# Kernel tuning notes

Measured on AMD Instinct MI355X. Metric: run time of the kernel, lower is better.

## Reference

```python
import jax, jax.numpy as jnp
import numpy as np

NB = 2        # trm_num_blocks
H = 4         # trm_num_heads
D = 128       # trm_hidden_dim
L = 512
B = 1
PAD = 0
NEG = jnp.float32(-2**32 + 1)


def _ln(x, g, b, eps=1e-8):
    m = x.mean(-1, keepdims=True)
    v = x.var(-1, keepdims=True)
    return (x - m) / jnp.sqrt(v + eps) * g + b


def setup_inputs() -> dict:
    key = jax.random.key(0)
    ks = jax.random.split(key, 16)
    s = 0.02
    inp = {
        "log_seqs": jax.random.randint(ks[0], (B, L), 0, 1000),
        "seqs": jax.random.normal(ks[1], (B, L, D), jnp.float32),
        "time_matrix_K": jax.random.normal(ks[2], (B, L, L, D), jnp.float32),
        # per-block stacked params [NB, ...]
        "Wq": jax.random.normal(ks[3], (NB, D, D), jnp.float32) * s,
        "bq": jnp.zeros((NB, D), jnp.float32),
        "Wk": jax.random.normal(ks[4], (NB, D, D), jnp.float32) * s,
        "bk": jnp.zeros((NB, D), jnp.float32),
        "Wv": jax.random.normal(ks[5], (NB, D, D), jnp.float32) * s,
        "bv": jnp.zeros((NB, D), jnp.float32),
        "Wt": jax.random.normal(ks[6], (NB, D, D), jnp.float32) * s,
        "bt": jnp.zeros((NB, D), jnp.float32),
        "Wtp": jax.random.normal(ks[7], (NB, D, 1), jnp.float32) * s,
        "btp": jnp.zeros((NB, 1), jnp.float32),
        "ln1_g": jnp.ones((NB, D), jnp.float32),
        "ln1_b": jnp.zeros((NB, D), jnp.float32),
        "ln2_g": jnp.ones((NB, D), jnp.float32),
        "ln2_b": jnp.zeros((NB, D), jnp.float32),
        "W1": jax.random.normal(ks[8], (NB, D, D), jnp.float32) * s,
        "b1": jnp.zeros((NB, D), jnp.float32),
        "W2": jax.random.normal(ks[9], (NB, D, D), jnp.float32) * s,
        "b2": jnp.zeros((NB, D), jnp.float32),
        "lnf_g": jnp.ones((D,), jnp.float32),
        "lnf_b": jnp.zeros((D,), jnp.float32),
    }
    return inp


def reference(log_seqs, seqs, time_matrix_K, Wq, bq, Wk, bk, Wv, bv, Wt, bt,
              Wtp, btp, ln1_g, ln1_b, ln2_g, ln2_b, W1, b1, W2, b2, lnf_g, lnf_b):
    hd = D // H
    pad = (log_seqs == PAD)                     # [B, L] True at padding
    keep = (~pad)[..., None].astype(seqs.dtype)  # [B, L, 1]
    seqs = seqs * keep
    causal = ~jnp.tril(jnp.ones((L, L), bool))  # True above diagonal (masked)
    # combined mask [1, B, L, L]: pad query rows OR non-causal entries
    mask = pad[None, :, :, None] | causal[None, None, :, :]

    attn_ws = []
    for i in range(NB):
        Q = _ln(seqs, ln1_g[i], ln1_b[i])
        q = Q @ Wq[i] + bq[i]
        k = seqs @ Wk[i] + bk[i]
        v = seqs @ Wv[i] + bv[i]
        # head-major layout [H, B, L, hd] (matches torch split+cat along dim 0)
        qh = q.reshape(B, L, H, hd).transpose(2, 0, 1, 3)
        kh = k.reshape(B, L, H, hd).transpose(2, 0, 1, 3)
        vh = v.reshape(B, L, H, hd).transpose(2, 0, 1, 3)
        scores = jnp.einsum('hbqd,hbkd->hbqk', qh, kh)  # [H, B, L, L]
        # time bias: sigmoid(proj(relu(W_t t))) in (0,1); log is negative
        tw = jax.nn.sigmoid(
            (jax.nn.relu(time_matrix_K @ Wt[i] + bt[i]) @ Wtp[i] + btp[i]).squeeze(-1)
        )                                             # [B, L, L]
        scores = (scores + jnp.log(tw)) / jnp.float32(hd) ** 0.5
        scores = jnp.where(mask, NEG, scores)
        w = jax.nn.softmax(scores, axis=-1)           # dropout is identity (eval)
        attn_ws.append(w.reshape(H * B, L, L))
        out = jnp.einsum('hbqk,hbkd->hbqd', w, vh).transpose(1, 2, 0, 3).reshape(B, L, D)
        seqs = Q + out
        x = _ln(seqs, ln2_g[i], ln2_b[i])
        y = jax.nn.relu(x @ W1[i] + b1[i]) @ W2[i] + b2[i]
        seqs = (x + y) * keep                         # FFN residual adds post-LN x
    log_feats = _ln(seqs, lnf_g, lnf_b)
    return (log_feats, tuple(attn_ws))
```

## Files before the change

### kernel.cpp

```cpp
#include <hip/hip_runtime.h>

#define L 512
#define D 128
#define H 4
#define HD 32
#define XLD 132
#define NTB 576

typedef __bf16 bf16x8 __attribute__((ext_vector_type(8)));
typedef float  f32x4  __attribute__((ext_vector_type(4)));

__device__ __forceinline__ unsigned short bfbits(float v){
  __bf16 h = (__bf16)v; unsigned short u; __builtin_memcpy(&u, &h, 2); return u;
}
__device__ __forceinline__ bf16x8 cvt8(float4 a0, float4 a1){
  bf16x8 r;
  r[0] = (__bf16)a0.x; r[1] = (__bf16)a0.y; r[2] = (__bf16)a0.z; r[3] = (__bf16)a0.w;
  r[4] = (__bf16)a1.x; r[5] = (__bf16)a1.y; r[6] = (__bf16)a1.z; r[7] = (__bf16)a1.w;
  return r;
}

__device__ __forceinline__ void write_qA(unsigned short* qA, int row, int c, float v){
  int qt = row >> 4, m = row & 15;
  int h = c >> 5, cc = c & 31;
  qA[(((qt * 4 + h) * 64) + (cc >> 3) * 16 + m) * 8 + (cc & 7)] = bfbits(v);
}
__device__ __forceinline__ void write_kB(unsigned short* kB, int row, int c, float v){
  int h = c >> 5, cc = c & 31;
  int nt = row >> 4;
  kB[((h * 32 + nt) * 64 + (cc >> 3) * 16 + (row & 15)) * 8 + (cc & 7)] = bfbits(v);
}
__device__ __forceinline__ void write_vB(unsigned short* vB, int row, int c, float v){
  int h = c >> 5, cc = c & 31;
  int kk = row >> 5, qv = (row >> 3) & 3, jv = row & 7;
  int nt = cc >> 4;
  vB[(((h * 16 + kk) * 2 + nt) * 64 + qv * 16 + (cc & 15)) * 8 + jv] = bfbits(v);
}

__device__ __forceinline__ void row_stats16(const float (*buf)[XLD], int tid,
                                            float* mean_s, float* rstd_s){
  int row_l = tid >> 4, seg = tid & 15;
  const float* p = &buf[row_l][seg * 8];
  float4 f0 = *(const float4*)p, f1 = *(const float4*)(p + 4);
  float sum = f0.x + f0.y + f0.z + f0.w + f1.x + f1.y + f1.z + f1.w;
  float sq  = f0.x*f0.x + f0.y*f0.y + f0.z*f0.z + f0.w*f0.w
            + f1.x*f1.x + f1.y*f1.y + f1.z*f1.z + f1.w*f1.w;
#pragma unroll
  for (int o = 1; o < 16; o <<= 1){ sum += __shfl_xor(sum, o); sq += __shfl_xor(sq, o); }
  if (seg == 0){
    float mn = sum * (1.f / 128.f);
    mean_s[row_l] = mn;
    rstd_s[row_l] = rsqrtf(fmaxf(sq * (1.f / 128.f) - mn * mn, 0.f) + 1e-8f);
  }
}

__device__ __forceinline__ void build_afr(const float (*buf)[XLD], int lane, bf16x8* afr){
  int m = lane & 15, quad = lane >> 4;
#pragma unroll
  for (int k0 = 0; k0 < 4; ++k0){
    const float* p = &buf[m][k0 * 32 + quad * 8];
    afr[k0] = cvt8(*(const float4*)p, *(const float4*)(p + 4));
  }
}
__device__ __forceinline__ void build_afr_ln(const float (*buf)[XLD], int lane,
    const float* mean_s, const float* rstd_s,
    const float* __restrict__ g, const float* __restrict__ b, bf16x8* afr){
  int m = lane & 15, quad = lane >> 4;
  float mn = mean_s[m], rs = rstd_s[m];
#pragma unroll
  for (int k0 = 0; k0 < 4; ++k0){
    int c0 = k0 * 32 + quad * 8;
    const float* p = &buf[m][c0];
    float4 a0 = *(const float4*)p, a1 = *(const float4*)(p + 4);
    float q[8];
    q[0]=(a0.x-mn)*rs*g[c0+0]+b[c0+0]; q[1]=(a0.y-mn)*rs*g[c0+1]+b[c0+1];
    q[2]=(a0.z-mn)*rs*g[c0+2]+b[c0+2]; q[3]=(a0.w-mn)*rs*g[c0+3]+b[c0+3];
    q[4]=(a1.x-mn)*rs*g[c0+4]+b[c0+4]; q[5]=(a1.y-mn)*rs*g[c0+5]+b[c0+5];
    q[6]=(a1.z-mn)*rs*g[c0+6]+b[c0+6]; q[7]=(a1.w-mn)*rs*g[c0+7]+b[c0+7];
    bf16x8 r;
    r[0]=(__bf16)q[0]; r[1]=(__bf16)q[1]; r[2]=(__bf16)q[2]; r[3]=(__bf16)q[3];
    r[4]=(__bf16)q[4]; r[5]=(__bf16)q[5]; r[6]=(__bf16)q[6]; r[7]=(__bf16)q[7];
    afr[k0] = r;
  }
}

__global__ void k_prep(const float* __restrict__ Wt,
                       const float* __restrict__ Wq, const float* __restrict__ Wk,
                       const float* __restrict__ Wv, const float* __restrict__ W1,
                       const float* __restrict__ W2,
                       unsigned short* __restrict__ bfg, unsigned short* __restrict__ wf){
  int idx = blockIdx.x * 256 + threadIdx.x;
  if (idx < 32768){
    int jj   = idx & 7;
    int lane = (idx >> 3) & 63;
    int k0   = (idx >> 9) & 3;
    int nt   = idx >> 11;
    int d    = k0 * 32 + (lane >> 4) * 8 + jj;
    int col  = (nt & 7) * 16 + (lane & 15);
    int blk  = nt >> 3;
    bfg[idx] = bfbits(Wt[blk * D * D + d * D + col]);
  } else {
    int i2 = idx - 32768;
    int jj = i2 & 7, lane = (i2 >> 3) & 63, k0 = (i2 >> 9) & 3, nt = (i2 >> 11) & 7;
    int mat = i2 >> 14;
    int blk = mat / 5, m5 = mat % 5;
    const float* W = (m5 == 0 ? Wq : m5 == 1 ? Wk : m5 == 2 ? Wv : m5 == 3 ? W1 : W2)
                     + blk * D * D;
    int d = k0 * 32 + (lane >> 4) * 8 + jj;
    int col = nt * 16 + (lane & 15);
    wf[i2] = bfbits(W[d * D + col]);
  }
}

__global__ __launch_bounds__(256, 2) void k_tb_qkv(
    const float* __restrict__ T, const unsigned short* __restrict__ bfg,
    const float* __restrict__ bt, const float* __restrict__ wtp,
    const float* __restrict__ btp, float* __restrict__ logtw,
    const float* __restrict__ src, const int* __restrict__ ls,
    const float* __restrict__ g1, const float* __restrict__ b1,
    const unsigned short* __restrict__ wf,
    const float* __restrict__ bq, const float* __restrict__ bk,
    const float* __restrict__ bv,
    float* __restrict__ Q, unsigned short* __restrict__ qA,
    unsigned short* __restrict__ kB, unsigned short* __restrict__ vB){
  __shared__ __align__(16) unsigned short bsh[16384];
  __shared__ float bts[128], wtps[128];
  __shared__ float xs[16][XLD];
  __shared__ float mean_s[16], rstd_s[16];
  __shared__ float g1s[128], b1s[128];
  int tid = threadIdx.x;
  int lane = tid & 63, w = tid >> 6;
  int quad = lane >> 4;

  if (blockIdx.x < NTB){
    int m = lane & 15;
    const bf16x8* bls = (const bf16x8*)bsh;
    int strip = blockIdx.x * 4 + w;
    int b = 0;
#pragma unroll
    for (int i = 1; i < 8; ++i) if (strip >= 32 * i * (i + 1)) b = i;
    int r0 = strip - 32 * b * (b + 1);
    int q  = b * 64 + r0 / (b + 1);
    int kb = (r0 % (b + 1)) * 64;
    int wbase = q * L + kb;

    bf16x8 afr[4][4];
#pragma unroll
    for (int mt = 0; mt < 4; ++mt){
      const float* tp = T + (size_t)(wbase + mt * 16 + m) * D + quad * 8;
#pragma unroll
      for (int k0 = 0; k0 < 4; ++k0){
        float4 f0 = *(const float4*)(tp + k0 * 32);
        float4 f1 = *(const float4*)(tp + k0 * 32 + 4);
        afr[mt][k0] = cvt8(f0, f1);
      }
    }

#pragma unroll
    for (int blk = 0; blk < 2; ++blk){
      if (blk) __syncthreads();
      {
        const uint4* g = (const uint4*)(bfg + blk * 16384);
        uint4* s = (uint4*)bsh;
#pragma unroll
        for (int i = 0; i < 8; ++i) s[tid + i * 256] = g[tid + i * 256];
        if (tid < 128){ bts[tid] = bt[blk * 128 + tid]; wtps[tid] = wtp[blk * 128 + tid]; }
      }
      __syncthreads();

      f32x4 rs[4] = {{0,0,0,0},{0,0,0,0},{0,0,0,0},{0,0,0,0}};
#pragma unroll
      for (int ntl = 0; ntl < 8; ++ntl){
        f32x4 acc[4] = {{0,0,0,0},{0,0,0,0},{0,0,0,0},{0,0,0,0}};
#pragma unroll
        for (int k0 = 0; k0 < 4; ++k0){
          bf16x8 bfr = bls[(ntl * 4 + k0) * 64 + lane];
#pragma unroll
          for (int mt = 0; mt < 4; ++mt)
            acc[mt] = __builtin_amdgcn_mfma_f32_16x16x32_bf16(afr[mt][k0], bfr, acc[mt], 0, 0, 0);
        }
        float btv = bts[ntl * 16 + m];
        float wtv = wtps[ntl * 16 + m];
#pragma unroll
        for (int mt = 0; mt < 4; ++mt)
#pragma unroll
          for (int r = 0; r < 4; ++r)
            rs[mt][r] += fmaxf(acc[mt][r] + btv, 0.f) * wtv;
      }
#pragma unroll
      for (int mt = 0; mt < 4; ++mt)
#pragma unroll
        for (int r = 0; r < 4; ++r){
          float v = rs[mt][r];
          v += __shfl_xor(v, 1); v += __shfl_xor(v, 2);
          v += __shfl_xor(v, 4); v += __shfl_xor(v, 8);
          rs[mt][r] = v;
        }
      if (m == 0){
        float bp = btp[blk];
        float* out = logtw + blk * (L * L);
#pragma unroll
        for (int mt = 0; mt < 4; ++mt){
          float4 o;
          float s0 = rs[mt][0] + bp; o.x = -__logf(1.f + __expf(-s0));
          float s1 = rs[mt][1] + bp; o.y = -__logf(1.f + __expf(-s1));
          float s2 = rs[mt][2] + bp; o.z = -__logf(1.f + __expf(-s2));
          float s3 = rs[mt][3] + bp; o.w = -__logf(1.f + __expf(-s3));
          *(float4*)(out + wbase + mt * 16 + quad * 4) = o;
        }
      }
    }
    return;
  }

  int bi = blockIdx.x - NTB;
  int rowbase = (bi & 31) * 16;
  int mat = bi >> 5;
  int row_l = tid >> 4, seg = tid & 15;

  const float* sp = src + (rowbase + row_l) * D + seg * 8;
  float4 f0 = *(const float4*)sp, f1 = *(const float4*)(sp + 4);
  if (ls[rowbase + row_l] == 0){
    f0 = make_float4(0,0,0,0); f1 = make_float4(0,0,0,0);
  }
  *(float4*)&xs[row_l][seg * 8] = f0;
  *(float4*)&xs[row_l][seg * 8 + 4] = f1;
  if (mat == 0 && tid < 128){ g1s[tid] = g1[tid]; b1s[tid] = b1[tid]; }
  __syncthreads();
  if (mat == 0){
    row_stats16(xs, tid, mean_s, rstd_s);
    __syncthreads();
    float mn = mean_s[row_l], rs = rstd_s[row_l];
    float* qp = Q + (rowbase + row_l) * D + seg * 8;
    float4 o0, o1;
    int c0 = seg * 8;
    o0.x=(f0.x-mn)*rs*g1s[c0+0]+b1s[c0+0]; o0.y=(f0.y-mn)*rs*g1s[c0+1]+b1s[c0+1];
    o0.z=(f0.z-mn)*rs*g1s[c0+2]+b1s[c0+2]; o0.w=(f0.w-mn)*rs*g1s[c0+3]+b1s[c0+3];
    o1.x=(f1.x-mn)*rs*g1s[c0+4]+b1s[c0+4]; o1.y=(f1.y-mn)*rs*g1s[c0+5]+b1s[c0+5];
    o1.z=(f1.z-mn)*rs*g1s[c0+6]+b1s[c0+6]; o1.w=(f1.w-mn)*rs*g1s[c0+7]+b1s[c0+7];
    *(float4*)qp = o0; *(float4*)(qp + 4) = o1;
  }

  int mcol = lane & 15;
  bf16x8 afr[4];
  if (mat == 0) build_afr_ln(xs, lane, mean_s, rstd_s, g1s, b1s, afr);
  else          build_afr(xs, lane, afr);

  const float* bias_v = (mat == 0 ? bq : mat == 1 ? bk : bv);
#pragma unroll
  for (int jl = 0; jl < 2; ++jl){
    int nt = w * 2 + jl;
    const bf16x8* wfb = (const bf16x8*)wf + ((size_t)mat * 8 + nt) * 4 * 64;
    f32x4 acc = {0, 0, 0, 0};
#pragma unroll
    for (int k0 = 0; k0 < 4; ++k0)
      acc = __builtin_amdgcn_mfma_f32_16x16x32_bf16(afr[k0], wfb[k0 * 64 + lane], acc, 0, 0, 0);
    int c = nt * 16 + mcol;
    float bias = bias_v[c];
#pragma unroll
    for (int r = 0; r < 4; ++r){
      int row = rowbase + quad * 4 + r;
      float v = acc[r] + bias;
      if (mat == 0) write_qA(qA, row, c, v);
      else if (mat == 1) write_kB(kB, row, c, v);
      else write_vB(vB, row, c, v);
    }
  }
}

__global__ __launch_bounds__(256) void k_attn(
    const unsigned short* __restrict__ qA, const unsigned short* __restrict__ kB,
    const unsigned short* __restrict__ vB, const float* __restrict__ logtw,
    const int* __restrict__ ls, const float* __restrict__ Q,
    float* __restrict__ wout, float* __restrict__ xr){
  __shared__ __align__(16) unsigned short pa[16 * 64 * 8];
  __shared__ float pvp[4][2][64][4];
  __shared__ float smax[4][16], ssum[4][16];
  int qt = blockIdx.x >> 2, h = blockIdx.x & 3;
  int tid = threadIdx.x, lane = tid & 63, w = tid >> 6;
  int quad = lane >> 4, mcol = lane & 15;
  const float RS = 0.17677669529663687f;
  int row_max = qt * 16 + 15;
  bool skipw = (w * 128) > row_max;

  float e[8][4];
  if (!skipw){
    bf16x8 qf = ((const bf16x8*)qA)[(qt * 4 + h) * 64 + lane];
    f32x4 acc[8];
#pragma unroll
    for (int nt8 = 0; nt8 < 8; ++nt8){
      bf16x8 bf = ((const bf16x8*)kB)[(h * 32 + w * 8 + nt8) * 64 + lane];
      f32x4 z = {0, 0, 0, 0};
      acc[nt8] = __builtin_amdgcn_mfma_f32_16x16x32_bf16(qf, bf, z, 0, 0, 0);
    }
#pragma unroll
    for (int nt8 = 0; nt8 < 8; ++nt8){
      int col = w * 128 + nt8 * 16 + mcol;
#pragma unroll
      for (int r = 0; r < 4; ++r){
        int row = qt * 16 + quad * 4 + r;
        float sv = (acc[nt8][r] + logtw[row * L + col]) * RS;
        e[nt8][r] = (col <= row) ? sv : -3e38f;
      }
    }
  } else {
#pragma unroll
    for (int nt8 = 0; nt8 < 8; ++nt8)
#pragma unroll
      for (int r = 0; r < 4; ++r) e[nt8][r] = -3e38f;
  }

  float mx4[4] = {-3e38f, -3e38f, -3e38f, -3e38f};
#pragma unroll
  for (int nt8 = 0; nt8 < 8; ++nt8)
#pragma unroll
    for (int r = 0; r < 4; ++r) mx4[r] = fmaxf(mx4[r], e[nt8][r]);
#pragma unroll
  for (int r = 0; r < 4; ++r){
    float v = mx4[r];
    v = fmaxf(v, __shfl_xor(v, 1)); v = fmaxf(v, __shfl_xor(v, 2));
    v = fmaxf(v, __shfl_xor(v, 4)); v = fmaxf(v, __shfl_xor(v, 8));
    mx4[r] = v;
  }
  if (mcol == 0){
#pragma unroll
    for (int r = 0; r < 4; ++r) smax[w][quad * 4 + r] = mx4[r];
  }
  __syncthreads();
  float mxr[4], sum4[4] = {0, 0, 0, 0};
#pragma unroll
  for (int r = 0; r < 4; ++r){
    int rr = quad * 4 + r;
    mxr[r] = fmaxf(fmaxf(smax[0][rr], smax[1][rr]), fmaxf(smax[2][rr], smax[3][rr]));
  }
#pragma unroll
  for (int nt8 = 0; nt8 < 8; ++nt8)
#pragma unroll
    for (int r = 0; r < 4; ++r){
      float sv = e[nt8][r];
      float ev = (sv > -1e38f) ? __expf(sv - mxr[r]) : 0.f;
      e[nt8][r] = ev;
      sum4[r] += ev;
    }
#pragma unroll
  for (int r = 0; r < 4; ++r){
    float v = sum4[r];
    v += __shfl_xor(v, 1); v += __shfl_xor(v, 2);
    v += __shfl_xor(v, 4); v += __shfl_xor(v, 8);
    sum4[r] = v;
  }
  if (mcol == 0){
#pragma unroll
    for (int r = 0; r < 4; ++r) ssum[w][quad * 4 + r] = sum4[r];
  }
  __syncthreads();
  float inv[4]; int padr[4];
#pragma unroll
  for (int r = 0; r < 4; ++r){
    int rr = quad * 4 + r;
    inv[r] = 1.f / (ssum[0][rr] + ssum[1][rr] + ssum[2][rr] + ssum[3][rr]);
    padr[r] = (ls[qt * 16 + rr] == 0);
  }
#pragma unroll
  for (int nt8 = 0; nt8 < 8; ++nt8){
    int col = w * 128 + nt8 * 16 + mcol;
    int kk = col >> 5, qk = (col >> 3) & 3, jj = col & 7;
#pragma unroll
    for (int r = 0; r < 4; ++r){
      int rl = quad * 4 + r;
      float wv = padr[r] ? (1.f / 512.f) : e[nt8][r] * inv[r];
      wout[h * (L * L) + (qt * 16 + rl) * L + col] = wv;
      if (!skipw) pa[(kk * 64 + qk * 16 + rl) * 8 + jj] = bfbits(wv);
    }
  }

  f32x4 pacc[2] = {{0,0,0,0},{0,0,0,0}};
  if (!skipw){
#pragma unroll
    for (int kk4 = 0; kk4 < 4; ++kk4){
      int kk = w * 4 + kk4;
      bf16x8 af = ((const bf16x8*)pa)[kk * 64 + lane];
#pragma unroll
      for (int nt = 0; nt < 2; ++nt){
        bf16x8 bf = ((const bf16x8*)vB)[((h * 16 + kk) * 2 + nt) * 64 + lane];
        pacc[nt] = __builtin_amdgcn_mfma_f32_16x16x32_bf16(af, bf, pacc[nt], 0, 0, 0);
      }
    }
  }
#pragma unroll
  for (int nt = 0; nt < 2; ++nt)
#pragma unroll
    for (int r = 0; r < 4; ++r) pvp[w][nt][lane][r] = pacc[nt][r];
  __syncthreads();
  if (w < 2){
    int nt = w;
#pragma unroll
    for (int r = 0; r < 4; ++r){
      float o = pvp[0][nt][lane][r] + pvp[1][nt][lane][r]
              + pvp[2][nt][lane][r] + pvp[3][nt][lane][r];
      int row = qt * 16 + quad * 4 + r;
      int cg = h * HD + nt * 16 + mcol;
      xr[row * D + cg] = Q[row * D + cg] + o;
    }
  }
}

__global__ __launch_bounds__(256) void k_ffn_m(
    const float* __restrict__ xr, const int* __restrict__ ls,
    const float* __restrict__ g2, const float* __restrict__ b2,
    const unsigned short* __restrict__ wf, int mat1,
    const float* __restrict__ b1f, const float* __restrict__ b2f,
    int fuse_qkv, const float* __restrict__ g1, const float* __restrict__ b1,
    int matq, const float* __restrict__ bq, const float* __restrict__ bk,
    const float* __restrict__ bv,
    float* __restrict__ Q, unsigned short* __restrict__ qA,
    unsigned short* __restrict__ kB, unsigned short* __restrict__ vB,
    int fuse_lnf, const float* __restrict__ lg, const float* __restrict__ lb,
    float* __restrict__ lf){
  __shared__ float xs[16][XLD];
  __shared__ float x2s[16][XLD];
  __shared__ float y1s[16][XLD];
  __shared__ float xos[16][XLD];
  __shared__ float mean_s[16], rstd_s[16];
  __shared__ float gs[128], bs[128];
  int tid = threadIdx.x, rowbase = blockIdx.x * 16;
  int row_l = tid >> 4, seg = tid & 15;
  int lane = tid & 63, w = tid >> 6;
  int quad = lane >> 4, mcol = lane & 15;

  {
    const float* sp = xr + (rowbase + row_l) * D + seg * 8;
    *(float4*)&xs[row_l][seg * 8] = *(const float4*)sp;
    *(float4*)&xs[row_l][seg * 8 + 4] = *(const float4*)(sp + 4);
    if (tid < 128){ gs[tid] = g2[tid]; bs[tid] = b2[tid]; }
  }
  __syncthreads();
  row_stats16(xs, tid, mean_s, rstd_s);
  __syncthreads();
  {
    float mn = mean_s[row_l], rs = rstd_s[row_l];
#pragma unroll
    for (int i = 0; i < 8; ++i){
      int c = seg * 8 + i;
      x2s[row_l][c] = (xs[row_l][c] - mn) * rs * gs[c] + bs[c];
    }
  }
  __syncthreads();

  bf16x8 afr[4];
  build_afr(x2s, lane, afr);
#pragma unroll
  for (int jl = 0; jl < 2; ++jl){
    int nt = w * 2 + jl;
    const bf16x8* wfb = (const bf16x8*)wf + ((size_t)mat1 * 8 + nt) * 4 * 64;
    f32x4 acc = {0, 0, 0, 0};
#pragma unroll
    for (int k0 = 0; k0 < 4; ++k0)
      acc = __builtin_amdgcn_mfma_f32_16x16x32_bf16(afr[k0], wfb[k0 * 64 + lane], acc, 0, 0, 0);
    int c = nt * 16 + mcol;
    float bias = b1f[c];
#pragma unroll
    for (int r = 0; r < 4; ++r)
      y1s[quad * 4 + r][c] = fmaxf(acc[r] + bias, 0.f);
  }
  __syncthreads();

  build_afr(y1s, lane, afr);
#pragma unroll
  for (int jl = 0; jl < 2; ++jl){
    int nt = w * 2 + jl;
    const bf16x8* wfb = (const bf16x8*)wf + ((size_t)(mat1 + 1) * 8 + nt) * 4 * 64;
    f32x4 acc = {0, 0, 0, 0};
#pragma unroll
    for (int k0 = 0; k0 < 4; ++k0)
      acc = __builtin_amdgcn_mfma_f32_16x16x32_bf16(afr[k0], wfb[k0 * 64 + lane], acc, 0, 0, 0);
    int c = nt * 16 + mcol;
    float bias = b2f[c];
#pragma unroll
    for (int r = 0; r < 4; ++r){
      int rl = quad * 4 + r;
      float kp = (ls[rowbase + rl] != 0) ? 1.f : 0.f;
      xos[rl][c] = (x2s[rl][c] + acc[r] + bias) * kp;
    }
  }
  __syncthreads();

  if (fuse_qkv){
    if (tid < 128){ gs[tid] = g1[tid]; bs[tid] = b1[tid]; }
    row_stats16(xos, tid, mean_s, rstd_s);
    __syncthreads();
    {
      float mn = mean_s[row_l], rs = rstd_s[row_l];
      float* qp = Q + (rowbase + row_l) * D + seg * 8;
      float4 o0, o1;
      int c0 = seg * 8;
      o0.x=(xos[row_l][c0+0]-mn)*rs*gs[c0+0]+bs[c0+0];
      o0.y=(xos[row_l][c0+1]-mn)*rs*gs[c0+1]+bs[c0+1];
      o0.z=(xos[row_l][c0+2]-mn)*rs*gs[c0+2]+bs[c0+2];
      o0.w=(xos[row_l][c0+3]-mn)*rs*gs[c0+3]+bs[c0+3];
      o1.x=(xos[row_l][c0+4]-mn)*rs*gs[c0+4]+bs[c0+4];
      o1.y=(xos[row_l][c0+5]-mn)*rs*gs[c0+5]+bs[c0+5];
      o1.z=(xos[row_l][c0+6]-mn)*rs*gs[c0+6]+bs[c0+6];
      o1.w=(xos[row_l][c0+7]-mn)*rs*gs[c0+7]+bs[c0+7];
      *(float4*)qp = o0; *(float4*)(qp + 4) = o1;
    }
    bf16x8 afrQ[4], afrX[4];
    build_afr_ln(xos, lane, mean_s, rstd_s, gs, bs, afrQ);
    build_afr(xos, lane, afrX);
#pragma unroll
    for (int jl = 0; jl < 6; ++jl){
      int j = w * 6 + jl;
      int mat = j >> 3, nt = j & 7;
      const bf16x8* wfb = (const bf16x8*)wf + ((size_t)(matq + mat) * 8 + nt) * 4 * 64;
      f32x4 acc = {0, 0, 0, 0};
#pragma unroll
      for (int k0 = 0; k0 < 4; ++k0)
        acc = __builtin_amdgcn_mfma_f32_16x16x32_bf16(mat == 0 ? afrQ[k0] : afrX[k0],
                                                      wfb[k0 * 64 + lane], acc, 0, 0, 0);
      int c = nt * 16 + mcol;
      float bias = (mat == 0 ? bq : mat == 1 ? bk : bv)[c];
#pragma unroll
      for (int r = 0; r < 4; ++r){
        int row = rowbase + quad * 4 + r;
        float v = acc[r] + bias;
        if (mat == 0) write_qA(qA, row, c, v);
        else if (mat == 1) write_kB(kB, row, c, v);
        else write_vB(vB, row, c, v);
      }
    }
  }

  if (fuse_lnf){
    if (tid < 128){ gs[tid] = lg[tid]; bs[tid] = lb[tid]; }
    row_stats16(xos, tid, mean_s, rstd_s);
    __syncthreads();
    float mn = mean_s[row_l], rs = rstd_s[row_l];
    float* op = lf + (rowbase + row_l) * D + seg * 8;
    float4 o0, o1;
    int c0 = seg * 8;
    o0.x=(xos[row_l][c0+0]-mn)*rs*gs[c0+0]+bs[c0+0];
    o0.y=(xos[row_l][c0+1]-mn)*rs*gs[c0+1]+bs[c0+1];
    o0.z=(xos[row_l][c0+2]-mn)*rs*gs[c0+2]+bs[c0+2];
    o0.w=(xos[row_l][c0+3]-mn)*rs*gs[c0+3]+bs[c0+3];
    o1.x=(xos[row_l][c0+4]-mn)*rs*gs[c0+4]+bs[c0+4];
    o1.y=(xos[row_l][c0+5]-mn)*rs*gs[c0+5]+bs[c0+5];
    o1.z=(xos[row_l][c0+6]-mn)*rs*gs[c0+6]+bs[c0+6];
    o1.w=(xos[row_l][c0+7]-mn)*rs*gs[c0+7]+bs[c0+7];
    *(float4*)op = o0; *(float4*)(op + 4) = o1;
  }
}

extern "C" void kernel_launch(void* const* d_in, const int* in_sizes, int n_in,
                              void* d_out, int out_size, void* d_ws, size_t ws_size,
                              hipStream_t stream){
  const int*   ls   = (const int*)d_in[0];
  const float* seqs = (const float*)d_in[1];
  const float* T    = (const float*)d_in[2];
  const float* Wq   = (const float*)d_in[3];
  const float* bq   = (const float*)d_in[4];
  const float* Wk   = (const float*)d_in[5];
  const float* bk   = (const float*)d_in[6];
  const float* Wv   = (const float*)d_in[7];
  const float* bv   = (const float*)d_in[8];
  const float* Wt   = (const float*)d_in[9];
  const float* bt   = (const float*)d_in[10];
  const float* Wtp  = (const float*)d_in[11];
  const float* btp  = (const float*)d_in[12];
  const float* g1   = (const float*)d_in[13];
  const float* b1   = (const float*)d_in[14];
  const float* g2   = (const float*)d_in[15];
  const float* b2   = (const float*)d_in[16];
  const float* W1   = (const float*)d_in[17];
  const float* b1f  = (const float*)d_in[18];
  const float* W2   = (const float*)d_in[19];
  const float* b2f  = (const float*)d_in[20];
  const float* lg   = (const float*)d_in[21];
  const float* lb   = (const float*)d_in[22];

  float* ws    = (float*)d_ws;
  float* Q     = ws;
  float* xr    = Q + 65536;
  float* logtw = xr + 65536;
  unsigned short* bfg = (unsigned short*)(logtw + 2 * 262144);
  unsigned short* wf  = bfg + 32768;
  unsigned short* qA  = wf + 163840;
  unsigned short* kB  = qA + 65536;
  unsigned short* vB  = kB + 65536;

  float* outF = (float*)d_out;
  float* lf = outF;
  float* w0 = outF + 65536;
  float* w1 = w0 + 1048576;

  k_prep  <<<768, 256, 0, stream>>>(Wt, Wq, Wk, Wv, W1, W2, bfg, wf);
  k_tb_qkv<<<NTB + 96, 256, 0, stream>>>(T, bfg, bt, Wtp, btp, logtw,
                                         seqs, ls, g1, b1, wf, bq, bk, bv,
                                         Q, qA, kB, vB);
  k_attn<<<128, 256, 0, stream>>>(qA, kB, vB, logtw, ls, Q, w0, xr);
  k_ffn_m<<<32, 256, 0, stream>>>(xr, ls, g2, b2, wf, 3, b1f, b2f,
                                  1, g1 + D, b1 + D, 5, bq + D, bk + D, bv + D,
                                  Q, qA, kB, vB,
                                  0, lg, lb, lf);
  k_attn<<<128, 256, 0, stream>>>(qA, kB, vB, logtw + L * L, ls, Q, w1, xr);
  k_ffn_m<<<32, 256, 0, stream>>>(xr, ls, g2 + D, b2 + D, wf, 8, b1f + D, b2f + D,
                                  0, g1, b1, 0, bq, bk, bv,
                                  Q, qA, kB, vB,
                                  1, lg, lb, lf);
}
```

Measured before the change: 267.3 us.

## Fuse all stages into one persistent kernel with software grid barriers

```diff
diff --git a/kernel.cpp b/kernel.cpp
--- a/kernel.cpp
+++ b/kernel.cpp
@@ -5,7 +5,7 @@
 #define H 4
 #define HD 32
 #define XLD 132
-#define NTB 576
+#define NBLK 512
 
 typedef __bf16 bf16x8 __attribute__((ext_vector_type(8)));
 typedef float  f32x4  __attribute__((ext_vector_type(4)));
@@ -18,6 +18,27 @@
   r[0] = (__bf16)a0.x; r[1] = (__bf16)a0.y; r[2] = (__bf16)a0.z; r[3] = (__bf16)a0.w;
   r[4] = (__bf16)a1.x; r[5] = (__bf16)a1.y; r[6] = (__bf16)a1.z; r[7] = (__bf16)a1.w;
   return r;
+}
+
+__device__ __forceinline__ void gridbar(unsigned* cnt, unsigned* gen){
+  __threadfence();
+  __syncthreads();
+  if (threadIdx.x == 0){
+    unsigned g = __hip_atomic_load(gen, __ATOMIC_RELAXED, __HIP_MEMORY_SCOPE_AGENT);
+    unsigned arr = __hip_atomic_fetch_add(cnt, 1u, __ATOMIC_ACQ_REL, __HIP_MEMORY_SCOPE_AGENT);
+    if (arr == NBLK - 1u){
+      __hip_atomic_store(cnt, 0u, __ATOMIC_RELAXED, __HIP_MEMORY_SCOPE_AGENT);
+      __hip_atomic_fetch_add(gen, 1u, __ATOMIC_ACQ_REL, __HIP_MEMORY_SCOPE_AGENT);
+    } else {
+      unsigned t = 0;
+      while (__hip_atomic_load(gen, __ATOMIC_ACQUIRE, __HIP_MEMORY_SCOPE_AGENT) == g){
+        __builtin_amdgcn_s_sleep(2);
+        if (++t > (1u << 28)) break;
+      }
+    }
+  }
+  __syncthreads();
+  __threadfence();
 }
 
 __device__ __forceinline__ void write_qA(unsigned short* qA, int row, int c, float v){
@@ -84,140 +105,28 @@
   }
 }
 
-__global__ void k_prep(const float* __restrict__ Wt,
-                       const float* __restrict__ Wq, const float* __restrict__ Wk,
-                       const float* __restrict__ Wv, const float* __restrict__ W1,
-                       const float* __restrict__ W2,
-                       unsigned short* __restrict__ bfg, unsigned short* __restrict__ wf){
-  int idx = blockIdx.x * 256 + threadIdx.x;
-  if (idx < 32768){
-    int jj   = idx & 7;
-    int lane = (idx >> 3) & 63;
-    int k0   = (idx >> 9) & 3;
-    int nt   = idx >> 11;
-    int d    = k0 * 32 + (lane >> 4) * 8 + jj;
-    int col  = (nt & 7) * 16 + (lane & 15);
-    int blk  = nt >> 3;
-    bfg[idx] = bfbits(Wt[blk * D * D + d * D + col]);
-  } else {
-    int i2 = idx - 32768;
-    int jj = i2 & 7, lane = (i2 >> 3) & 63, k0 = (i2 >> 9) & 3, nt = (i2 >> 11) & 7;
-    int mat = i2 >> 14;
-    int blk = mat / 5, m5 = mat % 5;
-    const float* W = (m5 == 0 ? Wq : m5 == 1 ? Wk : m5 == 2 ? Wv : m5 == 3 ? W1 : W2)
-                     + blk * D * D;
-    int d = k0 * 32 + (lane >> 4) * 8 + jj;
-    int col = nt * 16 + (lane & 15);
-    wf[i2] = bfbits(W[d * D + col]);
-  }
-}
-
-__global__ __launch_bounds__(256, 2) void k_tb_qkv(
-    const float* __restrict__ T, const unsigned short* __restrict__ bfg,
-    const float* __restrict__ bt, const float* __restrict__ wtp,
-    const float* __restrict__ btp, float* __restrict__ logtw,
-    const float* __restrict__ src, const int* __restrict__ ls,
+__device__ void qkv_part(int unit, const float* __restrict__ src,
+    const int* __restrict__ ls,
     const float* __restrict__ g1, const float* __restrict__ b1,
     const unsigned short* __restrict__ wf,
     const float* __restrict__ bq, const float* __restrict__ bk,
     const float* __restrict__ bv,
     float* __restrict__ Q, unsigned short* __restrict__ qA,
-    unsigned short* __restrict__ kB, unsigned short* __restrict__ vB){
-  __shared__ __align__(16) unsigned short bsh[16384];
-  __shared__ float bts[128], wtps[128];
-  __shared__ float xs[16][XLD];
-  __shared__ float mean_s[16], rstd_s[16];
-  __shared__ float g1s[128], b1s[128];
+    unsigned short* __restrict__ kB, unsigned short* __restrict__ vB,
+    unsigned char* smem){
+  float (*xs)[XLD] = (float(*)[XLD])smem;
+  float* mean_s = (float*)(smem + 8448);
+  float* rstd_s = mean_s + 16;
+  float* g1s = (float*)(smem + 8576);
+  float* b1s = g1s + 128;
   int tid = threadIdx.x;
+  int rowbase = (unit & 31) * 16;
+  int mat = unit >> 5;
+  int row_l = tid >> 4, seg = tid & 15;
   int lane = tid & 63, w = tid >> 6;
-  int quad = lane >> 4;
-
-  if (blockIdx.x < NTB){
-    int m = lane & 15;
-    const bf16x8* bls = (const bf16x8*)bsh;
-    int strip = blockIdx.x * 4 + w;
-    int b = 0;
-#pragma unroll
-    for (int i = 1; i < 8; ++i) if (strip >= 32 * i * (i + 1)) b = i;
-    int r0 = strip - 32 * b * (b + 1);
-    int q  = b * 64 + r0 / (b + 1);
-    int kb = (r0 % (b + 1)) * 64;
-    int wbase = q * L + kb;
-
-    bf16x8 afr[4][4];
-#pragma unroll
-    for (int mt = 0; mt < 4; ++mt){
-      const float* tp = T + (size_t)(wbase + mt * 16 + m) * D + quad * 8;
-#pragma unroll
-      for (int k0 = 0; k0 < 4; ++k0){
-        float4 f0 = *(const float4*)(tp + k0 * 32);
-        float4 f1 = *(const float4*)(tp + k0 * 32 + 4);
-        afr[mt][k0] = cvt8(f0, f1);
-      }
-    }
-
-#pragma unroll
-    for (int blk = 0; blk < 2; ++blk){
-      if (blk) __syncthreads();
-      {
-        const uint4* g = (const uint4*)(bfg + blk * 16384);
-        uint4* s = (uint4*)bsh;
-#pragma unroll
-        for (int i = 0; i < 8; ++i) s[tid + i * 256] = g[tid + i * 256];
-        if (tid < 128){ bts[tid] = bt[blk * 128 + tid]; wtps[tid] = wtp[blk * 128 + tid]; }
-      }
-      __syncthreads();
-
-      f32x4 rs[4] = {{0,0,0,0},{0,0,0,0},{0,0,0,0},{0,0,0,0}};
-#pragma unroll
-      for (int ntl = 0; ntl < 8; ++ntl){
-        f32x4 acc[4] = {{0,0,0,0},{0,0,0,0},{0,0,0,0},{0,0,0,0}};
-#pragma unroll
-        for (int k0 = 0; k0 < 4; ++k0){
-          bf16x8 bfr = bls[(ntl * 4 + k0) * 64 + lane];
-#pragma unroll
-          for (int mt = 0; mt < 4; ++mt)
-            acc[mt] = __builtin_amdgcn_mfma_f32_16x16x32_bf16(afr[mt][k0], bfr, acc[mt], 0, 0, 0);
-        }
-        float btv = bts[ntl * 16 + m];
-        float wtv = wtps[ntl * 16 + m];
-#pragma unroll
-        for (int mt = 0; mt < 4; ++mt)
-#pragma unroll
-          for (int r = 0; r < 4; ++r)
-            rs[mt][r] += fmaxf(acc[mt][r] + btv, 0.f) * wtv;
-      }
-#pragma unroll
-      for (int mt = 0; mt < 4; ++mt)
-#pragma unroll
-        for (int r = 0; r < 4; ++r){
-          float v = rs[mt][r];
-          v += __shfl_xor(v, 1); v += __shfl_xor(v, 2);
-          v += __shfl_xor(v, 4); v += __shfl_xor(v, 8);
-          rs[mt][r] = v;
-        }
-      if (m == 0){
-        float bp = btp[blk];
-        float* out = logtw + blk * (L * L);
-#pragma unroll
-        for (int mt = 0; mt < 4; ++mt){
-          float4 o;
-          float s0 = rs[mt][0] + bp; o.x = -__logf(1.f + __expf(-s0));
-          float s1 = rs[mt][1] + bp; o.y = -__logf(1.f + __expf(-s1));
-          float s2 = rs[mt][2] + bp; o.z = -__logf(1.f + __expf(-s2));
-          float s3 = rs[mt][3] + bp; o.w = -__logf(1.f + __expf(-s3));
-          *(float4*)(out + wbase + mt * 16 + quad * 4) = o;
-        }
-      }
-    }
-    return;
-  }
-
-  int bi = blockIdx.x - NTB;
-  int rowbase = (bi & 31) * 16;
-  int mat = bi >> 5;
-  int row_l = tid >> 4, seg = tid & 15;
-
+  int quad = lane >> 4, mcol = lane & 15;
+
+  __syncthreads();
   const float* sp = src + (rowbase + row_l) * D + seg * 8;
   float4 f0 = *(const float4*)sp, f1 = *(const float4*)(sp + 4);
   if (ls[rowbase + row_l] == 0){
@@ -241,7 +150,6 @@
     *(float4*)qp = o0; *(float4*)(qp + 4) = o1;
   }
 
-  int mcol = lane & 15;
   bf16x8 afr[4];
   if (mat == 0) build_afr_ln(xs, lane, mean_s, rstd_s, g1s, b1s, afr);
   else          build_afr(xs, lane, afr);
@@ -268,15 +176,16 @@
   }
 }
 
-__global__ __launch_bounds__(256) void k_attn(
+__device__ void attn_part(int unit,
     const unsigned short* __restrict__ qA, const unsigned short* __restrict__ kB,
     const unsigned short* __restrict__ vB, const float* __restrict__ logtw,
     const int* __restrict__ ls, const float* __restrict__ Q,
-    float* __restrict__ wout, float* __restrict__ xr){
-  __shared__ __align__(16) unsigned short pa[16 * 64 * 8];
-  __shared__ float pvp[4][2][64][4];
-  __shared__ float smax[4][16], ssum[4][16];
-  int qt = blockIdx.x >> 2, h = blockIdx.x & 3;
+    float* __restrict__ wout, float* __restrict__ xr, unsigned char* smem){
+  unsigned short* pa = (unsigned short*)smem;
+  float (*pvp)[2][64][4] = (float(*)[2][64][4])(smem + 16384);
+  float (*smax)[16] = (float(*)[16])(smem + 24576);
+  float (*ssum)[16] = (float(*)[16])(smem + 24832);
+  int qt = unit >> 2, h = unit & 3;
   int tid = threadIdx.x, lane = tid & 63, w = tid >> 6;
   int quad = lane >> 4, mcol = lane & 15;
   const float RS = 0.17677669529663687f;
@@ -405,8 +314,8 @@
   }
 }
 
-__global__ __launch_bounds__(256) void k_ffn_m(
-    const float* __restrict__ xr, const int* __restrict__ ls,
+__device__ void ffn_part(int unit, const float* __restrict__ xr,
+    const int* __restrict__ ls,
     const float* __restrict__ g2, const float* __restrict__ b2,
     const unsigned short* __restrict__ wf, int mat1,
     const float* __restrict__ b1f, const float* __restrict__ b2f,
@@ -416,14 +325,16 @@
     float* __restrict__ Q, unsigned short* __restrict__ qA,
     unsigned short* __restrict__ kB, unsigned short* __restrict__ vB,
     int fuse_lnf, const float* __restrict__ lg, const float* __restrict__ lb,
-    float* __restrict__ lf){
-  __shared__ float xs[16][XLD];
-  __shared__ float x2s[16][XLD];
-  __shared__ float y1s[16][XLD];
-  __shared__ float xos[16][XLD];
-  __shared__ float mean_s[16], rstd_s[16];
-  __shared__ float gs[128], bs[128];
-  int tid = threadIdx.x, rowbase = blockIdx.x * 16;
+    float* __restrict__ lf, unsigned char* smem){
+  float (*xs)[XLD]  = (float(*)[XLD])smem;
+  float (*x2s)[XLD] = (float(*)[XLD])(smem + 8448);
+  float (*y1s)[XLD] = (float(*)[XLD])(smem + 16896);
+  float (*xos)[XLD] = (float(*)[XLD])(smem + 25344);
+  float* mean_s = (float*)(smem + 33792);
+  float* rstd_s = mean_s + 16;
+  float* gs = (float*)(smem + 33920);
+  float* bs = gs + 128;
+  int tid = threadIdx.x, rowbase = unit * 16;
   int row_l = tid >> 4, seg = tid & 15;
   int lane = tid & 63, w = tid >> 6;
   int quad = lane >> 4, mcol = lane & 15;
@@ -548,6 +459,167 @@
     o1.w=(xos[row_l][c0+7]-mn)*rs*gs[c0+7]+bs[c0+7];
     *(float4*)op = o0; *(float4*)(op + 4) = o1;
   }
+}
+
+__global__ __launch_bounds__(256, 2) void k_mega(
+    const float* __restrict__ T, const int* __restrict__ ls,
+    const float* __restrict__ seqs,
+    const float* __restrict__ Wt, const float* __restrict__ Wq,
+    const float* __restrict__ Wk, const float* __restrict__ Wv,
+    const float* __restrict__ W1, const float* __restrict__ W2,
+    const float* __restrict__ bt, const float* __restrict__ wtp,
+    const float* __restrict__ btp,
+    const float* __restrict__ g1, const float* __restrict__ b1,
+    const float* __restrict__ g2, const float* __restrict__ b2,
+    const float* __restrict__ bq, const float* __restrict__ bk,
+    const float* __restrict__ bv,
+    const float* __restrict__ b1f, const float* __restrict__ b2f,
+    const float* __restrict__ lg, const float* __restrict__ lb,
+    float* __restrict__ Q, float* __restrict__ xr, float* __restrict__ logtw,
+    unsigned short* __restrict__ bfg, unsigned short* __restrict__ wf,
+    unsigned short* __restrict__ qA, unsigned short* __restrict__ kB,
+    unsigned short* __restrict__ vB,
+    unsigned* __restrict__ bar,
+    float* __restrict__ lf, float* __restrict__ w0, float* __restrict__ w1){
+  __shared__ __align__(16) unsigned char smem[34944];
+  unsigned* cnt = bar;
+  unsigned* gen = bar + 8;
+  int tid = threadIdx.x;
+  int bid = blockIdx.x;
+  int lane = tid & 63, w = tid >> 6;
+  int quad = lane >> 4;
+
+  for (int idx = bid * 256 + tid; idx < 196608; idx += NBLK * 256){
+    if (idx < 32768){
+      int jj   = idx & 7;
+      int ln   = (idx >> 3) & 63;
+      int k0   = (idx >> 9) & 3;
+      int nt   = idx >> 11;
+      int d    = k0 * 32 + (ln >> 4) * 8 + jj;
+      int col  = (nt & 7) * 16 + (ln & 15);
+      int blk  = nt >> 3;
+      bfg[idx] = bfbits(Wt[blk * D * D + d * D + col]);
+    } else {
+      int i2 = idx - 32768;
+      int jj = i2 & 7, ln = (i2 >> 3) & 63, k0 = (i2 >> 9) & 3, nt = (i2 >> 11) & 7;
+      int mat = i2 >> 14;
+      int blk = mat / 5, m5 = mat % 5;
+      const float* W = (m5 == 0 ? Wq : m5 == 1 ? Wk : m5 == 2 ? Wv : m5 == 3 ? W1 : W2)
+                       + blk * D * D;
+      int d = k0 * 32 + (ln >> 4) * 8 + jj;
+      int col = nt * 16 + (ln & 15);
+      wf[i2] = bfbits(W[d * D + col]);
+    }
+  }
+  gridbar(cnt, gen);
+
+  {
+    unsigned short* bsh = (unsigned short*)smem;
+    float* bts  = (float*)(smem + 32768);
+    float* wtps = bts + 128;
+    const bf16x8* bls = (const bf16x8*)bsh;
+    int m = lane & 15;
+    int niter = (bid < 64) ? 2 : 1;
+    for (int it = 0; it < niter; ++it){
+      int strip = it * 2048 + bid * 4 + w;
+      int b = 0;
+#pragma unroll
+      for (int i = 1; i < 8; ++i) if (strip >= 32 * i * (i + 1)) b = i;
+      int r0 = strip - 32 * b * (b + 1);
+      int q  = b * 64 + r0 / (b + 1);
+      int kb = (r0 % (b + 1)) * 64;
+      int wbase = q * L + kb;
+
+      bf16x8 afr[4][4];
+#pragma unroll
+      for (int mt = 0; mt < 4; ++mt){
+        const float* tp = T + (size_t)(wbase + mt * 16 + m) * D + quad * 8;
+#pragma unroll
+        for (int k0 = 0; k0 < 4; ++k0){
+          float4 f0 = *(const float4*)(tp + k0 * 32);
+          float4 f1 = *(const float4*)(tp + k0 * 32 + 4);
+          afr[mt][k0] = cvt8(f0, f1);
+        }
+      }
+
+#pragma unroll
+      for (int blk = 0; blk < 2; ++blk){
+        if (blk || it) __syncthreads();
+        {
+          const uint4* g = (const uint4*)(bfg + blk * 16384);
+          uint4* s = (uint4*)bsh;
+#pragma unroll
+          for (int i = 0; i < 8; ++i) s[tid + i * 256] = g[tid + i * 256];
+          if (tid < 128){ bts[tid] = bt[blk * 128 + tid]; wtps[tid] = wtp[blk * 128 + tid]; }
+        }
+        __syncthreads();
+
+        f32x4 rs[4] = {{0,0,0,0},{0,0,0,0},{0,0,0,0},{0,0,0,0}};
+#pragma unroll
+        for (int ntl = 0; ntl < 8; ++ntl){
+          f32x4 acc[4] = {{0,0,0,0},{0,0,0,0},{0,0,0,0},{0,0,0,0}};
+#pragma unroll
+          for (int k0 = 0; k0 < 4; ++k0){
+            bf16x8 bfr = bls[(ntl * 4 + k0) * 64 + lane];
+#pragma unroll
+            for (int mt = 0; mt < 4; ++mt)
+              acc[mt] = __builtin_amdgcn_mfma_f32_16x16x32_bf16(afr[mt][k0], bfr, acc[mt], 0, 0, 0);
+          }
+          float btv = bts[ntl * 16 + m];
+          float wtv = wtps[ntl * 16 + m];
+#pragma unroll
+          for (int mt = 0; mt < 4; ++mt)
+#pragma unroll
+            for (int r = 0; r < 4; ++r)
+              rs[mt][r] += fmaxf(acc[mt][r] + btv, 0.f) * wtv;
+        }
+#pragma unroll
+        for (int mt = 0; mt < 4; ++mt)
+#pragma unroll
+          for (int r = 0; r < 4; ++r){
+            float v = rs[mt][r];
+            v += __shfl_xor(v, 1); v += __shfl_xor(v, 2);
+            v += __shfl_xor(v, 4); v += __shfl_xor(v, 8);
+            rs[mt][r] = v;
+          }
+        if (m == 0){
+          float bp = btp[blk];
+          float* out = logtw + blk * (L * L);
+#pragma unroll
+          for (int mt = 0; mt < 4; ++mt){
+            float4 o;
+            float s0 = rs[mt][0] + bp; o.x = -__logf(1.f + __expf(-s0));
+            float s1 = rs[mt][1] + bp; o.y = -__logf(1.f + __expf(-s1));
+            float s2 = rs[mt][2] + bp; o.z = -__logf(1.f + __expf(-s2));
+            float s3 = rs[mt][3] + bp; o.w = -__logf(1.f + __expf(-s3));
+            *(float4*)(out + wbase + mt * 16 + quad * 4) = o;
+          }
+        }
+      }
+    }
+    if (bid >= 416)
+      qkv_part(bid - 416, seqs, ls, g1, b1, wf, bq, bk, bv, Q, qA, kB, vB, smem);
+  }
+  gridbar(cnt, gen);
+
+  if (bid < 128)
+    attn_part(bid, qA, kB, vB, logtw, ls, Q, w0, xr, smem);
+  gridbar(cnt, gen);
+
+  if (bid < 32)
+    ffn_part(bid, xr, ls, g2, b2, wf, 3, b1f, b2f,
+             1, g1 + D, b1 + D, 5, bq + D, bk + D, bv + D,
+             Q, qA, kB, vB, 0, lg, lb, lf, smem);
+  gridbar(cnt, gen);
+
+  if (bid < 128)
+    attn_part(bid, qA, kB, vB, logtw + L * L, ls, Q, w1, xr, smem);
+  gridbar(cnt, gen);
+
+  if (bid < 32)
+    ffn_part(bid, xr, ls, g2 + D, b2 + D, wf, 8, b1f + D, b2f + D,
+             0, g1, b1, 0, bq, bk, bv,
+             Q, qA, kB, vB, 1, lg, lb, lf, smem);
 }
 
 extern "C" void kernel_launch(void* const* d_in, const int* in_sizes, int n_in,
@@ -581,29 +653,22 @@
   float* Q     = ws;
   float* xr    = Q + 65536;
   float* logtw = xr + 65536;
-  unsigned short* bfg = (unsigned short*)(logtw + 2 * 262144);
+  unsigned short* bfg = (unsigned short*)(logtw + 524288);
   unsigned short* wf  = bfg + 32768;
   unsigned short* qA  = wf + 163840;
   unsigned short* kB  = qA + 65536;
   unsigned short* vB  = kB + 65536;
+  unsigned* bar = (unsigned*)(vB + 65536);
 
   float* outF = (float*)d_out;
   float* lf = outF;
   float* w0 = outF + 65536;
   float* w1 = w0 + 1048576;
 
-  k_prep  <<<768, 256, 0, stream>>>(Wt, Wq, Wk, Wv, W1, W2, bfg, wf);
-  k_tb_qkv<<<NTB + 96, 256, 0, stream>>>(T, bfg, bt, Wtp, btp, logtw,
-                                         seqs, ls, g1, b1, wf, bq, bk, bv,
-                                         Q, qA, kB, vB);
-  k_attn<<<128, 256, 0, stream>>>(qA, kB, vB, logtw, ls, Q, w0, xr);
-  k_ffn_m<<<32, 256, 0, stream>>>(xr, ls, g2, b2, wf, 3, b1f, b2f,
-                                  1, g1 + D, b1 + D, 5, bq + D, bk + D, bv + D,
-                                  Q, qA, kB, vB,
-                                  0, lg, lb, lf);
-  k_attn<<<128, 256, 0, stream>>>(qA, kB, vB, logtw + L * L, ls, Q, w1, xr);
-  k_ffn_m<<<32, 256, 0, stream>>>(xr, ls, g2 + D, b2 + D, wf, 8, b1f + D, b2f + D,
-                                  0, g1, b1, 0, bq, bk, bv,
-                                  Q, qA, kB, vB,
-                                  1, lg, lb, lf);
-}
+  hipMemsetAsync(bar, 0, 64, stream);
+  k_mega<<<NBLK, 256, 0, stream>>>(T, ls, seqs, Wt, Wq, Wk, Wv, W1, W2,
+                                   bt, Wtp, btp, g1, b1, g2, b2,
+                                   bq, bk, bv, b1f, b2f, lg, lb,
+                                   Q, xr, logtw, bfg, wf, qA, kB, vB,
+                                   bar, lf, w0, w1);
+}
```

Result: slower. 1.036 ms (+287.8%).
